# Optimization experiments

Hardware: AMD Instinct MI355X
Metric: run time of the kernel (lower is better)

The kernel has to match this reference:

```python
import jax, jax.numpy as jnp
import numpy as np

N_NODES = 20000
N_EDGES = 320000
IN_F = 256
OUT_F = 256
EDGE_F = 256


def _mlp2(x, W1, b1, W2, b2):
    # MLPLayers(2, [d_in, 2*d_in, d_out]) = Linear -> ReLU -> Linear
    return jax.nn.relu(x @ W1 + b1) @ W2 + b2


def setup_inputs() -> dict:
    key = jax.random.key(0)
    ks = jax.random.split(key, 12)

    def lin(k, fan_in, shape):
        bound = 1.0 / np.sqrt(fan_in)
        return jax.random.uniform(k, shape, jnp.float32, -bound, bound)

    node_feat = jax.random.normal(ks[0], (N_NODES, IN_F), jnp.float32)
    edge_feat = jax.random.normal(ks[1], (N_EDGES, EDGE_F), jnp.float32)
    src = jax.random.randint(ks[2], (N_EDGES,), 0, N_NODES, jnp.int32)
    dst = jax.random.randint(ks[3], (N_EDGES,), 0, N_NODES, jnp.int32)

    # edge_mlp: edge_feats -> 2*edge_feats -> in_feats
    We1 = lin(ks[4], EDGE_F, (EDGE_F, 2 * EDGE_F))
    be1 = lin(ks[5], EDGE_F, (2 * EDGE_F,))
    We2 = lin(ks[6], 2 * EDGE_F, (2 * EDGE_F, IN_F))
    be2 = lin(ks[7], 2 * EDGE_F, (IN_F,))
    # node mlp: in_feats -> 2*in_feats -> out_feats
    Wn1 = lin(ks[8], IN_F, (IN_F, 2 * IN_F))
    bn1 = lin(ks[9], IN_F, (2 * IN_F,))
    Wn2 = lin(ks[10], 2 * IN_F, (2 * IN_F, OUT_F))
    bn2 = lin(ks[11], 2 * IN_F, (OUT_F,))
    eps = jnp.zeros((1,), jnp.float32)

    return {"node_feat": node_feat, "edge_feat": edge_feat, "src": src, "dst": dst,
            "We1": We1, "be1": be1, "We2": We2, "be2": be2,
            "Wn1": Wn1, "bn1": bn1, "Wn2": Wn2, "bn2": bn2, "eps": eps}


def reference(node_feat, edge_feat, src, dst, We1, be1, We2, be2, Wn1, bn1, Wn2, bn2, eps):
    e = _mlp2(edge_feat, We1, be1, We2, be2)            # [E, IN_F]
    msg = jax.nn.relu(node_feat[src] + e)               # gather-add-relu
    out_h = jax.ops.segment_sum(msg, dst, num_segments=N_NODES)  # [N, IN_F]
    out = _mlp2((1.0 + eps[0]) * node_feat + out_h, Wn1, bn1, Wn2, bn2)
    return out
```

## Files before the change

### kernel.cpp

```cpp
#include <hip/hip_runtime.h>

#define NN  20000
#define NE  320000
#define FIN 256
#define FH  512

typedef __attribute__((ext_vector_type(8))) short bf16x8;
typedef __attribute__((ext_vector_type(4))) float f32x4;

static __device__ __forceinline__ unsigned short f2b(float f) {
    union { float f; unsigned int i; } v; v.f = f;
    return (unsigned short)((v.i + 0x7fffu + ((v.i >> 16) & 1u)) >> 16);
}
static __device__ __forceinline__ f32x4 mfma16(bf16x8 a, bf16x8 b, f32x4 c) {
    return __builtin_amdgcn_mfma_f32_16x16x32_bf16(a, b, c, 0, 0, 0);
}

__global__ void transpose_f32_bf16(const float* __restrict__ src,
                                   unsigned short* __restrict__ dst, int R, int C) {
    __shared__ unsigned short t[32][33];
    const int tx  = threadIdx.x & 31;
    const int tyb = threadIdx.x >> 5;
    const int bx = blockIdx.x % (C >> 5);
    const int by = blockIdx.x / (C >> 5);
    #pragma unroll
    for (int j = 0; j < 4; ++j) {
        const int row = by * 32 + tyb * 4 + j;
        t[tyb * 4 + j][tx] = f2b(src[(size_t)row * C + bx * 32 + tx]);
    }
    __syncthreads();
    #pragma unroll
    for (int j = 0; j < 4; ++j) {
        const int c = bx * 32 + tyb * 4 + j;
        dst[(size_t)c * R + by * 32 + tx] = t[tx][tyb * 4 + j];
    }
}

__global__ void hist_dst(const int* __restrict__ dstI, int* __restrict__ cnt) {
    int e = blockIdx.x * 256 + threadIdx.x;
    if (e < NE) atomicAdd(&cnt[dstI[e]], 1);
}

__global__ void scan_excl(const int* __restrict__ cnt, int* __restrict__ cursor) {
    __shared__ int s[1024];
    const int t = threadIdx.x;
    const int lo = t * 20;
    const int hi = (lo + 20 < NN) ? lo + 20 : NN;
    int sum = 0;
    for (int i = lo; i < hi; ++i) sum += cnt[i];
    s[t] = sum;
    __syncthreads();
    for (int off = 1; off < 1024; off <<= 1) {
        int v = (t >= off) ? s[t - off] : 0;
        __syncthreads();
        s[t] += v;
        __syncthreads();
    }
    int base = (t > 0) ? s[t - 1] : 0;
    for (int i = lo; i < hi; ++i) { cursor[i] = base; base += cnt[i]; }
}

__global__ void scatter_perm(const int* __restrict__ dstI,
                             int* __restrict__ cursor, int* __restrict__ perm) {
    int e = blockIdx.x * 256 + threadIdx.x;
    if (e < NE) {
        int pos = atomicAdd(&cursor[dstI[e]], 1);
        perm[pos] = e;
    }
}

__global__ void __launch_bounds__(256, 2)
gine_edge(const float* __restrict__ edge_feat,
          const float* __restrict__ node_feat,
          const int* __restrict__ srcI,
          const int* __restrict__ dstI,
          const int* __restrict__ perm,
          const unsigned short* __restrict__ W1T,
          const float* __restrict__ b1,
          const unsigned short* __restrict__ W2T,
          const float* __restrict__ b2,
          float* __restrict__ out_h)
{
    __shared__ union {
        unsigned short Xs[64 * 264];
        unsigned short Hs[64 * 512];
        float          Msg[64 * 260];
    } sh;
    __shared__ int snS[64], dnS[64], eS[64];

    const int tid  = threadIdx.x;
    const int wave = tid >> 6;
    const int lane = tid & 63;
    const int quad = lane >> 4;
    const int ln   = lane & 15;
    const int e0   = blockIdx.x * 64;

    if (tid < 64) {
        const int e = perm[e0 + tid];
        eS[tid]  = e;
        snS[tid] = srcI[e];
        dnS[tid] = dstI[e];
    }
    __syncthreads();

    #pragma unroll
    for (int it = 0; it < 8; ++it) {
        const int chunk = tid + it * 256;
        const int row = chunk >> 5;
        const int c8  = (chunk & 31) << 3;
        const float* p = edge_feat + (size_t)eS[row] * FIN + c8;
        f32x4 o0 = *(const f32x4*)(p);
        f32x4 o1 = *(const f32x4*)(p + 4);
        bf16x8 pack;
        #pragma unroll
        for (int j = 0; j < 4; ++j) {
            pack[j]     = (short)f2b(o0[j]);
            pack[j + 4] = (short)f2b(o1[j]);
        }
        *(bf16x8*)(&sh.Xs[row * 264 + c8]) = pack;
    }
    __syncthreads();

    f32x4 zero4 = {0.f, 0.f, 0.f, 0.f};
    f32x4 acc1[4][8];
    #pragma unroll
    for (int rt = 0; rt < 4; ++rt)
        #pragma unroll
        for (int cw = 0; cw < 8; ++cw) acc1[rt][cw] = zero4;

    const unsigned short* bB = W1T + (wave * 128 + ln) * FIN + quad * 8;
    #pragma unroll
    for (int ks = 0; ks < 8; ++ks) {
        bf16x8 a[4], b[8];
        #pragma unroll
        for (int rt = 0; rt < 4; ++rt)
            a[rt] = *(const bf16x8*)(&sh.Xs[(rt * 16 + ln) * 264 + quad * 8 + ks * 32]);
        #pragma unroll
        for (int cw = 0; cw < 8; ++cw)
            b[cw] = *(const bf16x8*)(bB + cw * 16 * FIN + ks * 32);
        #pragma unroll
        for (int rt = 0; rt < 4; ++rt)
            #pragma unroll
            for (int cw = 0; cw < 8; ++cw)
                acc1[rt][cw] = mfma16(a[rt], b[cw], acc1[rt][cw]);
    }
    __syncthreads();

    #pragma unroll
    for (int cw = 0; cw < 8; ++cw) {
        const int n = wave * 128 + cw * 16 + ln;
        const float bias = b1[n];
        #pragma unroll
        for (int rt = 0; rt < 4; ++rt)
            #pragma unroll
            for (int r = 0; r < 4; ++r) {
                const int row = rt * 16 + quad * 4 + r;
                const float v = fmaxf(acc1[rt][cw][r] + bias, 0.f);
                sh.Hs[(row << 9) + (((n >> 3) ^ (row & 7)) << 3) + (n & 7)] = f2b(v);
            }
    }
    __syncthreads();

    f32x4 acc2[4][4];
    #pragma unroll
    for (int rt = 0; rt < 4; ++rt)
        #pragma unroll
        for (int cw = 0; cw < 4; ++cw) acc2[rt][cw] = zero4;

    #pragma unroll
    for (int ks = 0; ks < 16; ++ks) {
        const int kb = ks * 4 + quad;
        bf16x8 a[4], b[4];
        #pragma unroll
        for (int rt = 0; rt < 4; ++rt) {
            const int row = rt * 16 + ln;
            a[rt] = *(const bf16x8*)(&sh.Hs[(row << 9) + (((kb ^ (row & 7)) << 3))]);
        }
        #pragma unroll
        for (int cw = 0; cw < 4; ++cw)
            b[cw] = *(const bf16x8*)(W2T + (wave * 64 + cw * 16 + ln) * FH + kb * 8);
        #pragma unroll
        for (int rt = 0; rt < 4; ++rt)
            #pragma unroll
            for (int cw = 0; cw < 4; ++cw)
                acc2[rt][cw] = mfma16(a[rt], b[cw], acc2[rt][cw]);
    }
    __syncthreads();

    float biasv[4];
    #pragma unroll
    for (int cw = 0; cw < 4; ++cw)
        biasv[cw] = b2[wave * 64 + cw * 16 + ln];
    #pragma unroll
    for (int rt = 0; rt < 4; ++rt)
        #pragma unroll
        for (int r = 0; r < 4; ++r) {
            const int row = rt * 16 + quad * 4 + r;
            const int sn = snS[row];
            const float* nf = node_feat + (size_t)sn * FIN + wave * 64 + ln;
            #pragma unroll
            for (int cw = 0; cw < 4; ++cw) {
                const float e = acc2[rt][cw][r] + biasv[cw];
                sh.Msg[row * 260 + wave * 64 + cw * 16 + ln] =
                    fmaxf(nf[cw * 16] + e, 0.f);
            }
        }
    __syncthreads();

    {
        const int col = tid;
        float run = sh.Msg[col];
        int cur = dnS[0];
        #pragma unroll 4
        for (int row = 1; row < 64; ++row) {
            const int d = dnS[row];
            if (d != cur) {
                atomicAdd(&out_h[(size_t)cur * FIN + col], run);
                run = 0.f;
                cur = d;
            }
            run += sh.Msg[row * 260 + col];
        }
        atomicAdd(&out_h[(size_t)cur * FIN + col], run);
    }
}

__global__ void __launch_bounds__(256, 2)
gine_node(const float* __restrict__ node_feat,
          const float* __restrict__ out_h,
          const unsigned short* __restrict__ W1T,
          const float* __restrict__ b1,
          const unsigned short* __restrict__ W2T,
          const float* __restrict__ b2,
          const float* __restrict__ eps,
          float* __restrict__ out)
{
    __shared__ union {
        unsigned short Xs[64 * 264];
        unsigned short Hs[64 * 512];
    } sh;

    const int tid  = threadIdx.x;
    const int wave = tid >> 6;
    const int lane = tid & 63;
    const int quad = lane >> 4;
    const int ln   = lane & 15;
    const int n0   = blockIdx.x * 64;
    const float epsv = 1.0f + eps[0];

    #pragma unroll
    for (int it = 0; it < 8; ++it) {
        const int chunk = tid + it * 256;
        const int row = chunk >> 5;
        const int c8  = (chunk & 31) << 3;
        const int g   = n0 + row;
        bf16x8 pack = {0, 0, 0, 0, 0, 0, 0, 0};
        if (g < NN) {
            const float* pn = node_feat + (size_t)g * FIN + c8;
            const float* ph = out_h + (size_t)g * FIN + c8;
            f32x4 n0v = *(const f32x4*)(pn);
            f32x4 n1v = *(const f32x4*)(pn + 4);
            f32x4 h0v = *(const f32x4*)(ph);
            f32x4 h1v = *(const f32x4*)(ph + 4);
            #pragma unroll
            for (int j = 0; j < 4; ++j) {
                pack[j]     = (short)f2b(epsv * n0v[j] + h0v[j]);
                pack[j + 4] = (short)f2b(epsv * n1v[j] + h1v[j]);
            }
        }
        *(bf16x8*)(&sh.Xs[row * 264 + c8]) = pack;
    }
    __syncthreads();

    f32x4 zero4 = {0.f, 0.f, 0.f, 0.f};
    f32x4 acc1[4][8];
    #pragma unroll
    for (int rt = 0; rt < 4; ++rt)
        #pragma unroll
        for (int cw = 0; cw < 8; ++cw) acc1[rt][cw] = zero4;

    const unsigned short* bB = W1T + (wave * 128 + ln) * FIN + quad * 8;
    #pragma unroll
    for (int ks = 0; ks < 8; ++ks) {
        bf16x8 a[4], b[8];
        #pragma unroll
        for (int rt = 0; rt < 4; ++rt)
            a[rt] = *(const bf16x8*)(&sh.Xs[(rt * 16 + ln) * 264 + quad * 8 + ks * 32]);
        #pragma unroll
        for (int cw = 0; cw < 8; ++cw)
            b[cw] = *(const bf16x8*)(bB + cw * 16 * FIN + ks * 32);
        #pragma unroll
        for (int rt = 0; rt < 4; ++rt)
            #pragma unroll
            for (int cw = 0; cw < 8; ++cw)
                acc1[rt][cw] = mfma16(a[rt], b[cw], acc1[rt][cw]);
    }
    __syncthreads();

    #pragma unroll
    for (int cw = 0; cw < 8; ++cw) {
        const int n = wave * 128 + cw * 16 + ln;
        const float bias = b1[n];
        #pragma unroll
        for (int rt = 0; rt < 4; ++rt)
            #pragma unroll
            for (int r = 0; r < 4; ++r) {
                const int row = rt * 16 + quad * 4 + r;
                const float v = fmaxf(acc1[rt][cw][r] + bias, 0.f);
                sh.Hs[(row << 9) + (((n >> 3) ^ (row & 7)) << 3) + (n & 7)] = f2b(v);
            }
    }
    __syncthreads();

    f32x4 acc2[4][4];
    #pragma unroll
    for (int rt = 0; rt < 4; ++rt)
        #pragma unroll
        for (int cw = 0; cw < 4; ++cw) acc2[rt][cw] = zero4;

    #pragma unroll
    for (int ks = 0; ks < 16; ++ks) {
        const int kb = ks * 4 + quad;
        bf16x8 a[4], b[4];
        #pragma unroll
        for (int rt = 0; rt < 4; ++rt) {
            const int row = rt * 16 + ln;
            a[rt] = *(const bf16x8*)(&sh.Hs[(row << 9) + (((kb ^ (row & 7)) << 3))]);
        }
        #pragma unroll
        for (int cw = 0; cw < 4; ++cw)
            b[cw] = *(const bf16x8*)(W2T + (wave * 64 + cw * 16 + ln) * FH + kb * 8);
        #pragma unroll
        for (int rt = 0; rt < 4; ++rt)
            #pragma unroll
            for (int cw = 0; cw < 4; ++cw)
                acc2[rt][cw] = mfma16(a[rt], b[cw], acc2[rt][cw]);
    }

    float biasv[4];
    #pragma unroll
    for (int cw = 0; cw < 4; ++cw)
        biasv[cw] = b2[wave * 64 + cw * 16 + ln];
    #pragma unroll
    for (int rt = 0; rt < 4; ++rt)
        #pragma unroll
        for (int r = 0; r < 4; ++r) {
            const int row = rt * 16 + quad * 4 + r;
            const int g = n0 + row;
            if (g < NN) {
                #pragma unroll
                for (int cw = 0; cw < 4; ++cw)
                    out[(size_t)g * FIN + wave * 64 + cw * 16 + ln] =
                        acc2[rt][cw][r] + biasv[cw];
            }
        }
}

extern "C" void kernel_launch(void* const* d_in, const int* in_sizes, int n_in,
                              void* d_out, int out_size, void* d_ws, size_t ws_size,
                              hipStream_t stream) {
    const float* node_feat = (const float*)d_in[0];
    const float* edge_feat = (const float*)d_in[1];
    const int* srcI = (const int*)d_in[2];
    const int* dstI = (const int*)d_in[3];
    const float* We1 = (const float*)d_in[4];
    const float* be1 = (const float*)d_in[5];
    const float* We2 = (const float*)d_in[6];
    const float* be2 = (const float*)d_in[7];
    const float* Wn1 = (const float*)d_in[8];
    const float* bn1 = (const float*)d_in[9];
    const float* Wn2 = (const float*)d_in[10];
    const float* bn2 = (const float*)d_in[11];
    const float* eps = (const float*)d_in[12];

    char* ws = (char*)d_ws;
    float* out_h = (float*)ws;
    unsigned short* W1T  = (unsigned short*)(ws + 20480000);
    unsigned short* W2T  = W1T + 131072;
    unsigned short* Wn1T = W2T + 131072;
    unsigned short* Wn2T = Wn1T + 131072;
    int* cnt    = (int*)(ws + 20480000 + 4 * 262144);
    int* cursor = cnt + NN;
    int* perm   = cursor + NN;

    hipMemsetAsync(out_h, 0, (size_t)NN * FIN * sizeof(float), stream);
    hipMemsetAsync(cnt, 0, NN * sizeof(int), stream);

    transpose_f32_bf16<<<128, 256, 0, stream>>>(We1, W1T, FIN, FH);
    transpose_f32_bf16<<<128, 256, 0, stream>>>(We2, W2T, FH, FIN);
    transpose_f32_bf16<<<128, 256, 0, stream>>>(Wn1, Wn1T, FIN, FH);
    transpose_f32_bf16<<<128, 256, 0, stream>>>(Wn2, Wn2T, FH, FIN);

    hist_dst<<<(NE + 255) / 256, 256, 0, stream>>>(dstI, cnt);
    scan_excl<<<1, 1024, 0, stream>>>(cnt, cursor);
    scatter_perm<<<(NE + 255) / 256, 256, 0, stream>>>(dstI, cursor, perm);

    gine_edge<<<NE / 64, 256, 0, stream>>>(edge_feat, node_feat, srcI, dstI,
                                           perm, W1T, be1, W2T, be2, out_h);
    gine_node<<<(NN + 63) / 64, 256, 0, stream>>>(node_feat, out_h, Wn1T, bn1,
                                                  Wn2T, bn2, eps, (float*)d_out);
}
```

Measured before the change: 950.2 us.

## Merge weight transposes, swizzle edge block order, store interior segments non-atomically

Merges the four weight-transpose launches into a single kernel that picks its matrix from the block index. Remaps edge-block indices so consecutive block IDs stride across the sorted edge list. Writes segment sums for destination nodes that lie wholly inside one block with plain stores instead of atomics, keeping atomics only for the first and last segments, which may span blocks. Together these aim to cut launch overhead, contention between concurrent blocks, and atomic traffic. The plain-store path depends on the buffer being zeroed and on edges being sorted by destination.

```diff
diff --git a/kernel.cpp b/kernel.cpp
--- a/kernel.cpp
+++ b/kernel.cpp
@@ -16,24 +16,29 @@
     return __builtin_amdgcn_mfma_f32_16x16x32_bf16(a, b, c, 0, 0, 0);
 }
 
-__global__ void transpose_f32_bf16(const float* __restrict__ src,
-                                   unsigned short* __restrict__ dst, int R, int C) {
-    __shared__ unsigned short t[32][33];
+__global__ void prep_weights(const float* __restrict__ We1, const float* __restrict__ We2,
+                             const float* __restrict__ Wn1, const float* __restrict__ Wn2,
+                             unsigned short* __restrict__ W1T, unsigned short* __restrict__ W2T,
+                             unsigned short* __restrict__ Wn1T, unsigned short* __restrict__ Wn2T) {
+    const int m = blockIdx.x >> 7;
+    const int t = blockIdx.x & 127;
+    const float* src; unsigned short* dst; int R, C;
+    if      (m == 0) { src = We1; dst = W1T;  R = 256; C = 512; }
+    else if (m == 1) { src = We2; dst = W2T;  R = 512; C = 256; }
+    else if (m == 2) { src = Wn1; dst = Wn1T; R = 256; C = 512; }
+    else             { src = Wn2; dst = Wn2T; R = 512; C = 256; }
+    __shared__ unsigned short tl[32][33];
     const int tx  = threadIdx.x & 31;
     const int tyb = threadIdx.x >> 5;
-    const int bx = blockIdx.x % (C >> 5);
-    const int by = blockIdx.x / (C >> 5);
-    #pragma unroll
-    for (int j = 0; j < 4; ++j) {
-        const int row = by * 32 + tyb * 4 + j;
-        t[tyb * 4 + j][tx] = f2b(src[(size_t)row * C + bx * 32 + tx]);
-    }
-    __syncthreads();
-    #pragma unroll
-    for (int j = 0; j < 4; ++j) {
-        const int c = bx * 32 + tyb * 4 + j;
-        dst[(size_t)c * R + by * 32 + tx] = t[tx][tyb * 4 + j];
-    }
+    const int cb = C >> 5;
+    const int bx = t % cb, by = t / cb;
+    #pragma unroll
+    for (int j = 0; j < 4; ++j)
+        tl[tyb * 4 + j][tx] = f2b(src[(size_t)(by * 32 + tyb * 4 + j) * C + bx * 32 + tx]);
+    __syncthreads();
+    #pragma unroll
+    for (int j = 0; j < 4; ++j)
+        dst[(size_t)(bx * 32 + tyb * 4 + j) * R + by * 32 + tx] = tl[tx][tyb * 4 + j];
 }
 
 __global__ void hist_dst(const int* __restrict__ dstI, int* __restrict__ cnt) {
@@ -93,7 +98,8 @@
     const int lane = tid & 63;
     const int quad = lane >> 4;
     const int ln   = lane & 15;
-    const int e0   = blockIdx.x * 64;
+    const int bs   = (blockIdx.x & 7) * 625 + (blockIdx.x >> 3);
+    const int e0   = bs * 64;
 
     if (tid < 64) {
         const int e = perm[e0 + tid];
@@ -209,13 +215,17 @@
 
     {
         const int col = tid;
+        const int d0 = dnS[0], d63 = dnS[63];
         float run = sh.Msg[col];
-        int cur = dnS[0];
+        int cur = d0;
         #pragma unroll 4
         for (int row = 1; row < 64; ++row) {
             const int d = dnS[row];
             if (d != cur) {
-                atomicAdd(&out_h[(size_t)cur * FIN + col], run);
+                if (cur == d0 || cur == d63)
+                    atomicAdd(&out_h[(size_t)cur * FIN + col], run);
+                else
+                    out_h[(size_t)cur * FIN + col] = run;
                 run = 0.f;
                 cur = d;
             }
@@ -386,10 +396,7 @@
     hipMemsetAsync(out_h, 0, (size_t)NN * FIN * sizeof(float), stream);
     hipMemsetAsync(cnt, 0, NN * sizeof(int), stream);
 
-    transpose_f32_bf16<<<128, 256, 0, stream>>>(We1, W1T, FIN, FH);
-    transpose_f32_bf16<<<128, 256, 0, stream>>>(We2, W2T, FH, FIN);
-    transpose_f32_bf16<<<128, 256, 0, stream>>>(Wn1, Wn1T, FIN, FH);
-    transpose_f32_bf16<<<128, 256, 0, stream>>>(Wn2, Wn2T, FH, FIN);
+    prep_weights<<<512, 256, 0, stream>>>(We1, We2, Wn1, Wn2, W1T, W2T, Wn1T, Wn2T);
 
     hist_dst<<<(NE + 255) / 256, 256, 0, stream>>>(dstI, cnt);
     scan_excl<<<1, 1024, 0, stream>>>(cnt, cursor);
```

Result: no change. 944.1 us (-0.6%).
